# Performance work log

Hardware: AMD Instinct MI355X
Metric: run time of the kernel (lower is better)

The kernel has to match this reference:

```python
import jax, jax.numpy as jnp
import numpy as np

DIM = 1024
HEADS = 16
DIM_HEAD = 64
INNER = HEADS * DIM_HEAD
SCALE = DIM_HEAD ** -0.5


def rotate_half(t):
    # '... (j d) -> ... j d' with j=2: split last dim in half
    x1, x2 = jnp.split(t, 2, axis=-1)
    return jnp.concatenate((-x2, x1), axis=-1)


def rotary_pos(n, d, dtype):
    inv_freq = 1.0 / (10000.0 ** (jnp.arange(0, d, 2, dtype=jnp.float32) / d))
    freqs = jnp.arange(n, dtype=jnp.float32)[:, None] * inv_freq[None, :]  # (n, d/2)
    return jnp.concatenate((freqs, freqs), axis=-1).astype(dtype)  # (n, d)


def apply_rope(pos, t):
    return t * jnp.cos(pos) + rotate_half(t) * jnp.sin(pos)


def setup_inputs() -> dict:
    key = jax.random.key(0)
    ks = jax.random.split(key, 5)
    x = jax.random.normal(ks[0], (2, 2048, DIM), dtype=jnp.float32)
    gamma = jnp.ones((DIM,), dtype=jnp.float32)
    beta = jnp.zeros((DIM,), dtype=jnp.float32)
    Wq = jax.random.normal(ks[1], (DIM, INNER), dtype=jnp.float32) * 0.02
    Wkv = jax.random.normal(ks[2], (DIM, 2 * INNER), dtype=jnp.float32) * 0.02
    Wo = jax.random.normal(ks[3], (INNER, DIM), dtype=jnp.float32) * 0.02
    return {"x": x, "gamma": gamma, "beta": beta, "Wq": Wq, "Wkv": Wkv, "Wo": Wo}


def reference(x, gamma, beta, Wq, Wkv, Wo):
    b, n, _ = x.shape
    # LayerNorm with learned gamma, fixed-zero beta buffer
    mu = jnp.mean(x, axis=-1, keepdims=True)
    var = jnp.var(x, axis=-1, keepdims=True)
    xn = (x - mu) / jnp.sqrt(var + 1e-5) * gamma + beta

    q = xn @ Wq                       # (b, n, inner)
    kv = xn @ Wkv
    k, v = jnp.split(kv, 2, axis=-1)

    def to_heads(t):
        return t.reshape(b, n, HEADS, DIM_HEAD).transpose(0, 2, 1, 3)  # b h n d

    q, k, v = map(to_heads, (q, k, v))

    pos = rotary_pos(n, DIM_HEAD, x.dtype)  # (n, d)
    q = apply_rope(pos, q)
    k = apply_rope(pos, k)

    q = q * SCALE
    sim = jnp.einsum('bhid,bhjd->bhij', q, k)

    neg = -jnp.finfo(sim.dtype).max
    causal_mask = jnp.triu(jnp.ones((n, n), dtype=bool), k=1)
    sim = jnp.where(causal_mask, neg, sim)

    attn = jax.nn.softmax(sim, axis=-1)
    out = jnp.einsum('bhij,bhjd->bhid', attn, v)
    out = out.transpose(0, 2, 1, 3).reshape(b, n, INNER)
    return out @ Wo
```

## Files before the change

kernel.cpp:

```cpp
#include <hip/hip_runtime.h>
#include <stdint.h>

typedef unsigned short u16;
typedef __attribute__((ext_vector_type(8))) short short8;
typedef __attribute__((ext_vector_type(4))) float floatx4;
typedef __attribute__((ext_vector_type(4))) unsigned short u16x4;
typedef __attribute__((ext_vector_type(2))) unsigned int uint2v;

__device__ __forceinline__ float bf2f(u16 v) {
  union { uint32_t u; float f; } x; x.u = ((uint32_t)v) << 16; return x.f;
}
__device__ __forceinline__ u16 f2bf(float f) {
  union { float f; uint32_t u; } x; x.f = f;
  uint32_t r = x.u + 0x7fffu + ((x.u >> 16) & 1u);
  return (u16)(r >> 16);
}
__device__ __forceinline__ uint32_t fu(float f) {
  union { float f; uint32_t u; } x; x.f = f; return x.u;
}

#define GL2LDS(g, l)                                                          \
  __builtin_amdgcn_global_load_lds(                                           \
      (const __attribute__((address_space(1))) void*)(g),                     \
      (__attribute__((address_space(3))) void*)(l), 16, 0, 0)

#define WAITBAR(N)                                                            \
  asm volatile("s_waitcnt vmcnt(" #N ")\n\ts_barrier" ::: "memory")
#define BARX asm volatile("s_barrier" ::: "memory")
#define VM0BARX asm volatile("s_waitcnt vmcnt(0)\n\ts_barrier" ::: "memory")

__global__ __launch_bounds__(256) void prep_k(const float* __restrict__ x,
                                              const float* __restrict__ gamma,
                                              const float* __restrict__ beta,
                                              const float* __restrict__ Wq,
                                              const float* __restrict__ Wkv,
                                              const float* __restrict__ Wo,
                                              u16* __restrict__ xn,
                                              u16* __restrict__ wqkvT,
                                              u16* __restrict__ woT) {
  int bid = blockIdx.x;
  int t = threadIdx.x;
  if (bid < 4096) {
    int row = bid;
    const float* xr = x + (size_t)row * 1024;
    float4 xv = *(const float4*)(xr + t * 4);
    float v0 = xv.x, v1 = xv.y, v2 = xv.z, v3 = xv.w;
    float s = v0 + v1 + v2 + v3;
    float s2 = v0 * v0 + v1 * v1 + v2 * v2 + v3 * v3;
#pragma unroll
    for (int d = 1; d < 64; d <<= 1) {
      s += __shfl_xor(s, d, 64);
      s2 += __shfl_xor(s2, d, 64);
    }
    __shared__ float red[8];
    int lane = t & 63, wv = t >> 6;
    if (lane == 0) { red[wv] = s; red[4 + wv] = s2; }
    __syncthreads();
    s = red[0] + red[1] + red[2] + red[3];
    s2 = red[4] + red[5] + red[6] + red[7];
    float mu = s * (1.0f / 1024.0f);
    float var = s2 * (1.0f / 1024.0f) - mu * mu;
    float rstd = rsqrtf(var + 1e-5f);
    float4 gv = *(const float4*)(gamma + t * 4);
    float4 bv = *(const float4*)(beta + t * 4);
    u16x4 ov;
    ov.x = f2bf((v0 - mu) * rstd * gv.x + bv.x);
    ov.y = f2bf((v1 - mu) * rstd * gv.y + bv.y);
    ov.z = f2bf((v2 - mu) * rstd * gv.z + bv.z);
    ov.w = f2bf((v3 - mu) * rstd * gv.w + bv.w);
    *(u16x4*)(xn + (size_t)row * 1024 + t * 4) = ov;
  } else {
    __shared__ u16 ldst[64][72];
    int wb = bid - 4096;
    const float* in;
    u16* outp;
    int C;
    if (wb < 256) { in = Wq; outp = wqkvT; C = 1024; }
    else if (wb < 768) { wb -= 256; in = Wkv; outp = wqkvT + 1024 * 1024; C = 2048; }
    else { wb -= 768; in = Wo; outp = woT; C = 1024; }
    int nbx = C >> 6;
    int c0 = (wb % nbx) * 64, r0 = (wb / nbx) * 64;
    int rt = t >> 2;
    int ci = (t & 3) * 16;
    const float* ip = in + (size_t)(r0 + rt) * C + c0 + ci;
#pragma unroll
    for (int q = 0; q < 4; q++) {
      float4 v = *(const float4*)(ip + q * 4);
      ldst[ci + q * 4 + 0][rt] = f2bf(v.x);
      ldst[ci + q * 4 + 1][rt] = f2bf(v.y);
      ldst[ci + q * 4 + 2][rt] = f2bf(v.z);
      ldst[ci + q * 4 + 3][rt] = f2bf(v.w);
    }
    __syncthreads();
    int ct = t >> 2;
    int ri = (t & 3) * 16;
    u16* op = outp + (size_t)(c0 + ct) * 1024 + r0 + ri;
    *(short8*)(op) = *(const short8*)&ldst[ct][ri];
    *(short8*)(op + 8) = *(const short8*)&ldst[ct][ri + 8];
  }
}

__global__ __launch_bounds__(512, 1) void gemm_qkv_k(const u16* __restrict__ A,
                                                     const u16* __restrict__ BT,
                                                     u16* __restrict__ C) {
  __shared__ __align__(16) u16 sA[2][128 * 64];
  __shared__ __align__(16) u16 sB[2][384 * 64];
  int tid = threadIdx.x;
  int w = tid >> 6, l = tid & 63;
  int lr = l & 15, lq = l >> 4;
  int wm = w >> 1, wn = w & 1;
  int bm = blockIdx.y * 128;
  int bn = blockIdx.x * 384;
  floatx4 acc[2][12] = {};
  int gcol = ((tid & 7) ^ ((tid >> 3) & 7)) * 8;
  int strow = tid >> 3;
  int t8 = tid * 8;
  const u16* gA = A + (size_t)(bm + strow) * 1024 + gcol;
  const u16* gB = BT + (size_t)(bn + strow) * 1024 + gcol;
  int csw = (lr & 7) << 3;
  int ar = (wm * 32 + lr) * 64;
  int br = (wn * 192 + lr) * 64;

#define ST_A(bi)                                                              \
  { GL2LDS(gA, &sA[bi][t8]); GL2LDS(gA + 65536, &sA[bi][t8 + 4096]); }
#define ST_B(bi)                                                              \
  { GL2LDS(gB, &sB[bi][t8]);                                                  \
    GL2LDS(gB + 65536, &sB[bi][t8 + 4096]);                                   \
    GL2LDS(gB + 131072, &sB[bi][t8 + 8192]);                                  \
    GL2LDS(gB + 196608, &sB[bi][t8 + 12288]);                                 \
    GL2LDS(gB + 262144, &sB[bi][t8 + 16384]);                                 \
    GL2LDS(gB + 327680, &sB[bi][t8 + 20480]); }
#define HALF(p, kh)                                                           \
  {                                                                           \
    int co_ = ((kh)*32 + lq * 8) ^ csw;                                       \
    short8 a0_ = *(const short8*)&sA[p][ar + co_];                            \
    short8 a1_ = *(const short8*)&sA[p][ar + 1024 + co_];                     \
    _Pragma("unroll") for (int g = 0; g < 3; g++) {                           \
      short8 b0_ = *(const short8*)&sB[p][br + (g * 4 + 0) * 1024 + co_];     \
      short8 b1_ = *(const short8*)&sB[p][br + (g * 4 + 1) * 1024 + co_];     \
      short8 b2_ = *(const short8*)&sB[p][br + (g * 4 + 2) * 1024 + co_];     \
      short8 b3_ = *(const short8*)&sB[p][br + (g * 4 + 3) * 1024 + co_];     \
      acc[0][g*4+0] = __builtin_amdgcn_mfma_f32_16x16x32_bf16(a0_, b0_, acc[0][g*4+0], 0, 0, 0); \
      acc[1][g*4+0] = __builtin_amdgcn_mfma_f32_16x16x32_bf16(a1_, b0_, acc[1][g*4+0], 0, 0, 0); \
      acc[0][g*4+1] = __builtin_amdgcn_mfma_f32_16x16x32_bf16(a0_, b1_, acc[0][g*4+1], 0, 0, 0); \
      acc[1][g*4+1] = __builtin_amdgcn_mfma_f32_16x16x32_bf16(a1_, b1_, acc[1][g*4+1], 0, 0, 0); \
      acc[0][g*4+2] = __builtin_amdgcn_mfma_f32_16x16x32_bf16(a0_, b2_, acc[0][g*4+2], 0, 0, 0); \
      acc[1][g*4+2] = __builtin_amdgcn_mfma_f32_16x16x32_bf16(a1_, b2_, acc[1][g*4+2], 0, 0, 0); \
      acc[0][g*4+3] = __builtin_amdgcn_mfma_f32_16x16x32_bf16(a0_, b3_, acc[0][g*4+3], 0, 0, 0); \
      acc[1][g*4+3] = __builtin_amdgcn_mfma_f32_16x16x32_bf16(a1_, b3_, acc[1][g*4+3], 0, 0, 0); \
    }                                                                         \
  }
#define KT(p, q, DOST)                                                        \
  {                                                                           \
    if (DOST) { ST_A(q); ST_B(q); gA += 64; gB += 64; }                       \
    BARX; __builtin_amdgcn_s_setprio(1);                                      \
    HALF(p, 0);                                                               \
    __builtin_amdgcn_s_setprio(0); BARX;                                      \
    __builtin_amdgcn_s_setprio(1);                                            \
    HALF(p, 1);                                                               \
    __builtin_amdgcn_s_setprio(0); VM0BARX;                                   \
  }

  ST_A(0); ST_B(0); gA += 64; gB += 64;
  VM0BARX;
#pragma unroll 1
  for (int t = 0; t < 7; ++t) {
    KT(0, 1, 1);
    KT(1, 0, 1);
  }
  KT(0, 1, 1);
  KT(1, 0, 0);

#pragma unroll
  for (int nig = 0; nig < 3; nig++) {
    int col0 = bn + wn * 192 + nig * 64;
    int sec = col0 >> 10;
    if (sec == 2) {
#pragma unroll
      for (int p4 = 0; p4 < 4; p4++) {
        int ni = nig * 4 + p4;
        int col = col0 + p4 * 16 + lr;
        int cv = col - 2048;
#pragma unroll
        for (int mi = 0; mi < 2; mi++) {
          int row = bm + wm * 32 + mi * 16 + lq * 4;
          int bq = row >> 11;
          int n = row & 2047;
          int bh = (bq << 4) | (cv >> 6);
          int d = cv & 63;
          size_t L = ((size_t)(bh * 64 + d) << 11) + n;
          u16x4 ov;
          ov.x = f2bf(acc[mi][ni][0]);
          ov.y = f2bf(acc[mi][ni][1]);
          ov.z = f2bf(acc[mi][ni][2]);
          ov.w = f2bf(acc[mi][ni][3]);
          *(u16x4*)(C + (L >> 10) * 3072 + 2048 + (L & 1023)) = ov;
        }
      }
    } else {
      float QS = (sec == 0) ? 0.125f * 1.44269504088896f : 1.0f;
#pragma unroll
      for (int np = 0; np < 2; np++) {
        int i = np * 16 + lr;
        float invf = exp2f(-(float)i * 0.4152410118609203f);
#pragma unroll
        for (int mi = 0; mi < 2; mi++)
#pragma unroll
          for (int r = 0; r < 4; r++) {
            int row = bm + wm * 32 + mi * 16 + lq * 4 + r;
            int n = row & 2047;
            float ang = (float)n * invf;
            float s_, c_;
            __sincosf(ang, &s_, &c_);
            float x1 = acc[mi][nig * 4 + np][r];
            float x2 = acc[mi][nig * 4 + np + 2][r];
            int col = col0 + np * 16 + lr;
            C[(size_t)row * 3072 + col] = f2bf((x1 * c_ - x2 * s_) * QS);
            C[(size_t)row * 3072 + col + 32] = f2bf((x2 * c_ + x1 * s_) * QS);
          }
      }
    }
  }
}

__global__ __launch_bounds__(512, 1) void gemm64_bf16_k(const u16* __restrict__ A,
                                                        const u16* __restrict__ BT,
                                                        float* __restrict__ C) {
  __shared__ __align__(16) u16 sA[2][128 * 64];
  __shared__ __align__(16) u16 sB[2][128 * 64];
  int tid = threadIdx.x;
  int w = tid >> 6, l = tid & 63;
  int lr = l & 15, lq = l >> 4;
  int wm = w >> 1, wn = w & 1;
  int bm = blockIdx.y * 128;
  int bn = blockIdx.x * 128;
  floatx4 acc[2][4] = {};
  int gcol = ((tid & 7) ^ ((tid >> 3) & 7)) * 8;
  int strow = tid >> 3;
  int t8 = tid * 8;
  const u16* gA = A + (size_t)(bm + strow) * 1024 + gcol;
  const u16* gB = BT + (size_t)(bn + strow) * 1024 + gcol;
  int csw = (lr & 7) << 3;
  int ar = (wm * 32 + lr) * 64;
  int br = (wn * 64 + lr) * 64;

#define ST_A2(bi)                                                             \
  { GL2LDS(gA, &sA[bi][t8]); GL2LDS(gA + 65536, &sA[bi][t8 + 4096]); }
#define ST_B2(bi)                                                             \
  { GL2LDS(gB, &sB[bi][t8]); GL2LDS(gB + 65536, &sB[bi][t8 + 4096]); }
#define HALF2(p, kh)                                                          \
  {                                                                           \
    int co_ = ((kh)*32 + lq * 8) ^ csw;                                       \
    short8 a0_ = *(const short8*)&sA[p][ar + co_];                            \
    short8 a1_ = *(const short8*)&sA[p][ar + 1024 + co_];                     \
    short8 b0_ = *(const short8*)&sB[p][br + 0 + co_];                        \
    short8 b1_ = *(const short8*)&sB[p][br + 1024 + co_];                     \
    short8 b2_ = *(const short8*)&sB[p][br + 2048 + co_];                     \
    short8 b3_ = *(const short8*)&sB[p][br + 3072 + co_];                     \
    acc[0][0] = __builtin_amdgcn_mfma_f32_16x16x32_bf16(a0_, b0_, acc[0][0], 0, 0, 0); \
    acc[1][0] = __builtin_amdgcn_mfma_f32_16x16x32_bf16(a1_, b0_, acc[1][0], 0, 0, 0); \
    acc[0][1] = __builtin_amdgcn_mfma_f32_16x16x32_bf16(a0_, b1_, acc[0][1], 0, 0, 0); \
    acc[1][1] = __builtin_amdgcn_mfma_f32_16x16x32_bf16(a1_, b1_, acc[1][1], 0, 0, 0); \
    acc[0][2] = __builtin_amdgcn_mfma_f32_16x16x32_bf16(a0_, b2_, acc[0][2], 0, 0, 0); \
    acc[1][2] = __builtin_amdgcn_mfma_f32_16x16x32_bf16(a1_, b2_, acc[1][2], 0, 0, 0); \
    acc[0][3] = __builtin_amdgcn_mfma_f32_16x16x32_bf16(a0_, b3_, acc[0][3], 0, 0, 0); \
    acc[1][3] = __builtin_amdgcn_mfma_f32_16x16x32_bf16(a1_, b3_, acc[1][3], 0, 0, 0); \
  }
#define KT2(p, q, DOST)                                                       \
  {                                                                           \
    if (DOST) { ST_A2(q); ST_B2(q); gA += 64; gB += 64; }                     \
    BARX; __builtin_amdgcn_s_setprio(1);                                      \
    HALF2(p, 0);                                                              \
    __builtin_amdgcn_s_setprio(0); BARX;                                      \
    __builtin_amdgcn_s_setprio(1);                                            \
    HALF2(p, 1);                                                              \
    __builtin_amdgcn_s_setprio(0); VM0BARX;                                   \
  }

  ST_A2(0); ST_B2(0); gA += 64; gB += 64;
  VM0BARX;
#pragma unroll 1
  for (int t = 0; t < 7; ++t) {
    KT2(0, 1, 1);
    KT2(1, 0, 1);
  }
  KT2(0, 1, 1);
  KT2(1, 0, 0);

#pragma unroll
  for (int mi = 0; mi < 2; mi++)
#pragma unroll
    for (int ni = 0; ni < 4; ni++) {
      int row = bm + wm * 32 + mi * 16 + lq * 4;
      int col = bn + wn * 64 + ni * 16 + lr;
#pragma unroll
      for (int r = 0; r < 4; r++)
        C[(size_t)(row + r) * 1024 + col] = acc[mi][ni][r];
    }
}

#define LPT 64
__device__ __forceinline__ void attn_tile2(const u16* lK, const u16* lV, u16* lp,
                                           const short8* aq, floatx4* o,
                                           float& l_i, int lr, int lq,
                                           bool diag, int q0, int k0g,
                                           short8 ones) {
  floatx4 s[4];
#pragma unroll
  for (int ni = 0; ni < 4; ni++) {
    floatx4 a = {};
#pragma unroll
    for (int kc = 0; kc < 2; kc++) {
      int R = ni * 16 + lr;
      int c8 = (kc * 4 + lq) ^ (R & 7);
      short8 kf = *(const short8*)&lK[R * 64 + c8 * 8];
      a = __builtin_amdgcn_mfma_f32_16x16x32_bf16(kf, aq[kc], a, 0, 0, 0);
    }
    s[ni] = a;
  }
  if (diag) {
    int qg = q0 + lr;
#pragma unroll
    for (int ni = 0; ni < 4; ni++)
#pragma unroll
      for (int r = 0; r < 4; r++) {
        int kg = k0g + ni * 16 + lq * 4 + r;
        if (kg > qg) s[ni][r] = -1e30f;
      }
  }
  int swz = (lr & 7) << 3;
#pragma unroll
  for (int ni = 0; ni < 4; ni++) {
    float p0 = exp2f(s[ni][0]), p1 = exp2f(s[ni][1]);
    float p2 = exp2f(s[ni][2]), p3 = exp2f(s[ni][3]);
    uint2v dw;
    dw.x = __builtin_amdgcn_perm(fu(p1), fu(p0), 0x07060302u);
    dw.y = __builtin_amdgcn_perm(fu(p3), fu(p2), 0x07060302u);
    *(uint2v*)&lp[lr * LPT + ((ni * 16 + lq * 4) ^ swz)] = dw;
  }
  short8 pb0 = *(const short8*)&lp[lr * LPT + ((lq * 8) ^ swz)];
  short8 pb1 = *(const short8*)&lp[lr * LPT + ((32 + lq * 8) ^ swz)];
  floatx4 z = {};
  z = __builtin_amdgcn_mfma_f32_16x16x32_bf16(ones, pb0, z, 0, 0, 0);
  z = __builtin_amdgcn_mfma_f32_16x16x32_bf16(ones, pb1, z, 0, 0, 0);
  l_i += z[0];
#pragma unroll
  for (int di = 0; di < 4; di++) {
    int R = di * 16 + lr;
    int c80 = lq ^ (R & 7);
    int c81 = (4 + lq) ^ (R & 7);
    short8 v0 = *(const short8*)&lV[R * 64 + c80 * 8];
    o[di] = __builtin_amdgcn_mfma_f32_16x16x32_bf16(v0, pb0, o[di], 0, 0, 0);
    short8 v1 = *(const short8*)&lV[R * 64 + c81 * 8];
    o[di] = __builtin_amdgcn_mfma_f32_16x16x32_bf16(v1, pb1, o[di], 0, 0, 0);
  }
}

__global__ __launch_bounds__(256) void attn_k(const u16* __restrict__ qkv,
                                              u16* __restrict__ out) {
  __shared__ __align__(16) u16 lK[2][64 * 64];
  __shared__ __align__(16) u16 lV[2][64 * 64];
  __shared__ __align__(16) u16 lP[4][16 * LPT];
  int bh = blockIdx.x;
  int b = bh >> 4, h = bh & 15;
  int y = blockIdx.y;
  int g = y >> 3, o_ = y & 7;
  int j = (g & 1) ? ((g << 3) + 7 - o_) : y;
  int tid = threadIdx.x;
  int w = tid >> 6, l = tid & 63;
  int lr = l & 15, lq = l >> 4;
  int q0 = j * 64 + w * 16;
  const u16* qb = qkv + (size_t)b * 2048 * 3072 + h * 64;
  const u16* kb = qkv + (size_t)b * 2048 * 3072 + 1024 + h * 64;
  int bh64 = bh * 64;
  short8 aq[2];
  aq[0] = *(const short8*)(qb + (size_t)(q0 + lr) * 3072 + lq * 8);
  aq[1] = *(const short8*)(qb + (size_t)(q0 + lr) * 3072 + 32 + lq * 8);
  short8 ones;
#pragma unroll
  for (int i = 0; i < 8; i++) ones[i] = (short)0x3F80;
  floatx4 o[4] = {};
  float l_ = 0.0f;
  int srow8 = l >> 3;
  int sc8 = (l & 7) ^ srow8;
  u16* lp = &lP[w][0];
  int row0 = w * 8 + srow8;
  int row1 = (w + 4) * 8 + srow8;
  const u16* kp0 = kb + (size_t)row0 * 3072 + sc8 * 8;
  const u16* kp1 = kb + (size_t)row1 * 3072 + sc8 * 8;
  const u16* vp0 = qkv + (size_t)((bh64 + row0) * 2) * 3072 + 2048 + sc8 * 8;
  const u16* vp1 = qkv + (size_t)((bh64 + row1) * 2) * 3072 + 2048 + sc8 * 8;
  auto stage = [&](int bufi) {
    GL2LDS(kp0, &lK[bufi][w * 512]);
    GL2LDS(vp0, &lV[bufi][w * 512]);
    GL2LDS(kp1, &lK[bufi][(w + 4) * 512]);
    GL2LDS(vp1, &lV[bufi][(w + 4) * 512]);
  };
  auto advance = [&](int ktStaged) {
    kp0 += 196608; kp1 += 196608;
    int dv = (((ktStaged + 1) & 15) == 0) ? 2112 : 64;
    vp0 += dv; vp1 += dv;
  };
  stage(0);
  advance(0);
  for (int kt = 0; kt <= j; ++kt) {
    int cur = kt & 1;
    __syncthreads();
    if (kt < j) { stage(cur ^ 1); advance(kt + 1); }
    attn_tile2(lK[cur], lV[cur], lp, aq, o, l_, lr, lq, kt == j, q0, kt * 64,
               ones);
  }
  float rl = 1.0f / l_;
#pragma unroll
  for (int di = 0; di < 4; di++) {
    uint2v dw;
    u16 a0 = f2bf(o[di][0] * rl), a1 = f2bf(o[di][1] * rl);
    u16 a2 = f2bf(o[di][2] * rl), a3 = f2bf(o[di][3] * rl);
    dw.x = (uint32_t)a0 | ((uint32_t)a1 << 16);
    dw.y = (uint32_t)a2 | ((uint32_t)a3 << 16);
    int dcol = h * 64 + di * 16 + lq * 4;
    *(uint2v*)(out + ((size_t)(b * 2048 + q0 + lr)) * 1024 + dcol) = dw;
  }
}

extern "C" void kernel_launch(void* const* d_in, const int* in_sizes, int n_in,
                              void* d_out, int out_size, void* d_ws, size_t ws_size,
                              hipStream_t stream) {
  const float* x = (const float*)d_in[0];
  const float* gamma = (const float*)d_in[1];
  const float* beta = (const float*)d_in[2];
  const float* Wq = (const float*)d_in[3];
  const float* Wkv = (const float*)d_in[4];
  const float* Wo = (const float*)d_in[5];
  float* out = (float*)d_out;
  char* ws = (char*)d_ws;

  u16* qkv = (u16*)(ws);
  u16* wqkvT = (u16*)(ws + 25165824);
  u16* woT = (u16*)(ws + 31457280);
  u16* xn = (u16*)(ws + 33554432);
  u16* attn_out = xn;

  prep_k<<<5120, 256, 0, stream>>>(x, gamma, beta, Wq, Wkv, Wo, xn, wqkvT, woT);
  gemm_qkv_k<<<dim3(8, 32), 512, 0, stream>>>(xn, wqkvT, qkv);
  attn_k<<<dim3(32, 32), 256, 0, stream>>>(qkv, attn_out);
  gemm64_bf16_k<<<dim3(8, 32), 512, 0, stream>>>(attn_out, woT, out);
}
```

Measured before the change: 181.5 us.

## Remap GEMM blocks per XCD for L2 locality; sum softmax denominators in fp32

Both GEMM kernels now launch a 1D grid and remap block IDs so each XCD (blocks assigned round-robin by id mod 8) works on a compact 8x4 tile region, aiming for better L2 reuse of A and B tiles. Separately, the attention kernel drops the two extra MFMAs with a ones vector that computed the row sum of P. Instead it accumulates the sum in fp32 scalars per lane and reduces across the four lane quads with shuffles at the end. The row sum is now taken from fp32 probabilities rather than the bf16-truncated values, which slightly changes numerics, and it adds a few VALU adds per tile.

```diff
diff --git a/kernel.cpp b/kernel.cpp
--- a/kernel.cpp
+++ b/kernel.cpp
@@ -28,6 +28,12 @@
   asm volatile("s_waitcnt vmcnt(" #N ")\n\ts_barrier" ::: "memory")
 #define BARX asm volatile("s_barrier" ::: "memory")
 #define VM0BARX asm volatile("s_waitcnt vmcnt(0)\n\ts_barrier" ::: "memory")
+
+__device__ __forceinline__ void xcd_remap(int bid, int& bmi, int& bni) {
+  int x = bid & 7, s = bid >> 3;
+  bmi = ((x >> 1) << 3) | (s & 7);
+  bni = ((x & 1) << 2) | (s >> 3);
+}
 
 __global__ __launch_bounds__(256) void prep_k(const float* __restrict__ x,
                                               const float* __restrict__ gamma,
@@ -109,8 +115,10 @@
   int w = tid >> 6, l = tid & 63;
   int lr = l & 15, lq = l >> 4;
   int wm = w >> 1, wn = w & 1;
-  int bm = blockIdx.y * 128;
-  int bn = blockIdx.x * 384;
+  int bmi, bni;
+  xcd_remap(blockIdx.x, bmi, bni);
+  int bm = bmi * 128;
+  int bn = bni * 384;
   floatx4 acc[2][12] = {};
   int gcol = ((tid & 7) ^ ((tid >> 3) & 7)) * 8;
   int strow = tid >> 3;
@@ -232,8 +240,10 @@
   int w = tid >> 6, l = tid & 63;
   int lr = l & 15, lq = l >> 4;
   int wm = w >> 1, wn = w & 1;
-  int bm = blockIdx.y * 128;
-  int bn = blockIdx.x * 128;
+  int bmi, bni;
+  xcd_remap(blockIdx.x, bmi, bni);
+  int bm = bmi * 128;
+  int bn = bni * 128;
   floatx4 acc[2][4] = {};
   int gcol = ((tid & 7) ^ ((tid >> 3) & 7)) * 8;
   int strow = tid >> 3;
@@ -303,8 +313,7 @@
 __device__ __forceinline__ void attn_tile2(const u16* lK, const u16* lV, u16* lp,
                                            const short8* aq, floatx4* o,
                                            float& l_i, int lr, int lq,
-                                           bool diag, int q0, int k0g,
-                                           short8 ones) {
+                                           bool diag, int q0, int k0g) {
   floatx4 s[4];
 #pragma unroll
   for (int ni = 0; ni < 4; ni++) {
@@ -333,6 +342,7 @@
   for (int ni = 0; ni < 4; ni++) {
     float p0 = exp2f(s[ni][0]), p1 = exp2f(s[ni][1]);
     float p2 = exp2f(s[ni][2]), p3 = exp2f(s[ni][3]);
+    l_i += (p0 + p1) + (p2 + p3);
     uint2v dw;
     dw.x = __builtin_amdgcn_perm(fu(p1), fu(p0), 0x07060302u);
     dw.y = __builtin_amdgcn_perm(fu(p3), fu(p2), 0x07060302u);
@@ -340,10 +350,6 @@
   }
   short8 pb0 = *(const short8*)&lp[lr * LPT + ((lq * 8) ^ swz)];
   short8 pb1 = *(const short8*)&lp[lr * LPT + ((32 + lq * 8) ^ swz)];
-  floatx4 z = {};
-  z = __builtin_amdgcn_mfma_f32_16x16x32_bf16(ones, pb0, z, 0, 0, 0);
-  z = __builtin_amdgcn_mfma_f32_16x16x32_bf16(ones, pb1, z, 0, 0, 0);
-  l_i += z[0];
 #pragma unroll
   for (int di = 0; di < 4; di++) {
     int R = di * 16 + lr;
@@ -376,9 +382,6 @@
   short8 aq[2];
   aq[0] = *(const short8*)(qb + (size_t)(q0 + lr) * 3072 + lq * 8);
   aq[1] = *(const short8*)(qb + (size_t)(q0 + lr) * 3072 + 32 + lq * 8);
-  short8 ones;
-#pragma unroll
-  for (int i = 0; i < 8; i++) ones[i] = (short)0x3F80;
   floatx4 o[4] = {};
   float l_ = 0.0f;
   int srow8 = l >> 3;
@@ -407,9 +410,10 @@
     int cur = kt & 1;
     __syncthreads();
     if (kt < j) { stage(cur ^ 1); advance(kt + 1); }
-    attn_tile2(lK[cur], lV[cur], lp, aq, o, l_, lr, lq, kt == j, q0, kt * 64,
-               ones);
-  }
+    attn_tile2(lK[cur], lV[cur], lp, aq, o, l_, lr, lq, kt == j, q0, kt * 64);
+  }
+  l_ += __shfl_xor(l_, 16, 64);
+  l_ += __shfl_xor(l_, 32, 64);
   float rl = 1.0f / l_;
 #pragma unroll
   for (int di = 0; di < 4; di++) {
@@ -442,7 +446,7 @@
   u16* attn_out = xn;
 
   prep_k<<<5120, 256, 0, stream>>>(x, gamma, beta, Wq, Wkv, Wo, xn, wqkvT, woT);
-  gemm_qkv_k<<<dim3(8, 32), 512, 0, stream>>>(xn, wqkvT, qkv);
+  gemm_qkv_k<<<256, 512, 0, stream>>>(xn, wqkvT, qkv);
   attn_k<<<dim3(32, 32), 256, 0, stream>>>(qkv, attn_out);
-  gemm64_bf16_k<<<dim3(8, 32), 512, 0, stream>>>(attn_out, woT, out);
-}
+  gemm64_bf16_k<<<256, 512, 0, stream>>>(attn_out, woT, out);
+}
```

New measurement: 178.9 us. No clear change (-1.4%).
